# Kernel optimization log

Hardware: AMD Instinct MI355X
Metric: run time of the kernel (lower is better)

Reference implementation:

```python
import jax, jax.numpy as jnp
import numpy as np

# Model config (mirrors Mamba2Block(dim=256) with mamba_ssm defaults)
D_MODEL = 256
EXPAND = 2
D_INNER = D_MODEL * EXPAND          # 512
HEADDIM = D_MODEL * EXPAND // 8     # 64
NHEADS = D_INNER // HEADDIM         # 8
D_STATE = 64
D_CONV = 4
CONV_DIM = D_INNER + 2 * D_STATE    # 640 (ngroups=1)
D_IN_PROJ = 2 * D_INNER + 2 * D_STATE + NHEADS  # 1160
BATCH, SEQLEN = 2, 2048
EPS = 1e-5


def setup_inputs() -> dict:
    key = jax.random.key(0)
    ks = jax.random.split(key, 12)
    s = 0.02
    return {
        "hidden_states": jax.random.normal(ks[0], (BATCH, SEQLEN, D_MODEL), jnp.float32),
        "norm_w": jnp.ones((D_MODEL,), jnp.float32),
        "norm_b": jnp.zeros((D_MODEL,), jnp.float32),
        "W_in": jax.random.normal(ks[1], (D_MODEL, D_IN_PROJ), jnp.float32) * s,
        "conv_w": jax.random.normal(ks[2], (CONV_DIM, D_CONV), jnp.float32) * 0.25,
        "conv_b": jnp.zeros((CONV_DIM,), jnp.float32),
        "dt_bias": jax.random.uniform(ks[3], (NHEADS,), jnp.float32),
        "A_log": jax.random.uniform(ks[4], (NHEADS,), jnp.float32),  # A = -exp(A_log) in (-e, -1]
        "D_param": jnp.ones((NHEADS,), jnp.float32),
        "rms_w": jnp.ones((D_INNER,), jnp.float32),
        "W_out": jax.random.normal(ks[5], (D_INNER, D_MODEL), jnp.float32) * s,
    }


def _layer_norm(x, w, b):
    mu = jnp.mean(x, -1, keepdims=True)
    var = jnp.mean((x - mu) ** 2, -1, keepdims=True)
    return (x - mu) * jax.lax.rsqrt(var + EPS) * w + b


def _causal_depthwise_conv(x, w, b):
    # x: [B,L,C], w: [C,K] depthwise causal conv
    B, L, C = x.shape
    K = w.shape[1]
    xp = jnp.pad(x, ((0, 0), (K - 1, 0), (0, 0)))
    y = b
    for k in range(K):  # K=4, fixed small kernel
        y = y + w[:, k] * xp[:, k:k + L, :]
    return y


def reference(hidden_states, norm_w, norm_b, W_in, conv_w, conv_b, dt_bias, A_log, D_param, rms_w, W_out):
    B, L, D = hidden_states.shape
    residual = hidden_states                       # residual is None, drop_path=0
    x = _layer_norm(residual, norm_w, norm_b)      # pre-norm

    zxbcdt = jnp.einsum("bld,de->ble", x, W_in)    # [B,L,2*Di+2*N+H]
    z = zxbcdt[..., :D_INNER]
    xBC = zxbcdt[..., D_INNER:D_INNER + CONV_DIM]
    dt = zxbcdt[..., -NHEADS:]

    xBC = jax.nn.silu(_causal_depthwise_conv(xBC, conv_w, conv_b))
    xs = xBC[..., :D_INNER]
    Bm = xBC[..., D_INNER:D_INNER + D_STATE]       # [B,L,N] (ngroups=1)
    Cm = xBC[..., D_INNER + D_STATE:]              # [B,L,N]

    dt = jax.nn.softplus(dt + dt_bias)             # [B,L,H]
    A = -jnp.exp(A_log)                            # [H]
    dA = jnp.exp(dt * A)                           # [B,L,H]

    xh = xs.reshape(B, L, NHEADS, HEADDIM)         # [B,L,H,P]
    dtx = dt[..., None] * xh                       # [B,L,H,P]

    def step(s, inp):
        dA_t, dtx_t, B_t, C_t = inp                # [B,H],[B,H,P],[B,N],[B,N]
        s = s * dA_t[:, :, None, None] + dtx_t[..., None] * B_t[:, None, None, :]
        y_t = jnp.einsum("bhpn,bn->bhp", s, C_t)
        return s, y_t

    s0 = jnp.zeros((B, NHEADS, HEADDIM, D_STATE), hidden_states.dtype)
    xs_in = (jnp.swapaxes(dA, 0, 1), jnp.swapaxes(dtx, 0, 1),
             jnp.swapaxes(Bm, 0, 1), jnp.swapaxes(Cm, 0, 1))
    _, ys = jax.lax.scan(step, s0, xs_in)          # ys: [L,B,H,P]
    y = jnp.swapaxes(ys, 0, 1) + D_param[None, None, :, None] * xh  # skip term
    y = y.reshape(B, L, D_INNER)

    # gated RMSNorm (norm_before_gate=False): rmsnorm(y * silu(z)) * rms_w
    g = y * jax.nn.silu(z)
    g = g * jax.lax.rsqrt(jnp.mean(g * g, -1, keepdims=True) + EPS) * rms_w

    out = jnp.einsum("bld,de->ble", g, W_out)
    return out, residual
```

## Files before the change

kernel.cpp:

```cpp
#include <hip/hip_runtime.h>
#include <hip/hip_bf16.h>

#define BATCH 2
#define SEQLEN 2048
#define DMODEL 256
#define DINNER 512
#define NHEADS 8
#define HEADDIM 64
#define DSTATE 64
#define CONVDIM 640
#define DINPROJ 1160
#define NTOK (BATCH*SEQLEN)
#define Q 64
#define NCH (SEQLEN/Q)
#define NPAD2 1280
#define TS 72
#define RS3 196

typedef short v8s __attribute__((ext_vector_type(8)));
typedef float v4f __attribute__((ext_vector_type(4)));

__device__ __forceinline__ unsigned short f2bf(float f){
    __hip_bfloat16 h = __float2bfloat16(f);
    return *reinterpret_cast<unsigned short*>(&h);
}
__device__ __forceinline__ float bf2f(unsigned short u){
    unsigned int x = ((unsigned int)u) << 16;
    return __uint_as_float(x);
}

__global__ __launch_bounds__(256) void k_prep(
        const float* __restrict__ hid, const float* __restrict__ nw, const float* __restrict__ nb,
        const float* __restrict__ Win, const float* __restrict__ Wout,
        float* __restrict__ res, unsigned short* __restrict__ Xb,
        unsigned short* __restrict__ Wti, unsigned short* __restrict__ Wto){
    int bx = blockIdx.x;
    int t = threadIdx.x;
    if(bx < 256){
        __shared__ float xs[16][DMODEL];
        int tok0 = bx*16;
        for(int i=0;i<16;i++){
            int idx = i*256+t; int j = idx>>8, c = idx&255;
            float v = hid[(size_t)(tok0+j)*DMODEL + c];
            xs[j][c] = v;
            res[(size_t)(tok0+j)*DMODEL + c] = v;
        }
        __syncthreads();
        int g = t>>4, il = t&15;
        float sum=0.f, sumsq=0.f;
        for(int i=0;i<16;i++){ float v = xs[g][il*16+i]; sum += v; sumsq += v*v; }
        #pragma unroll
        for(int m=1;m<16;m<<=1){ sum += __shfl_xor(sum,m); sumsq += __shfl_xor(sumsq,m); }
        float mu   = sum*(1.f/256.f);
        float var  = sumsq*(1.f/256.f) - mu*mu;
        float rstd = rsqrtf(var + 1e-5f);
        for(int i=0;i<16;i++){
            int c = il*16+i;
            xs[g][c] = (xs[g][c]-mu)*rstd*nw[c] + nb[c];
        }
        __syncthreads();
        for(int i=0;i<16;i++){
            int idx = i*256+t; int j = idx>>8, c = idx&255;
            Xb[(size_t)(tok0+j)*DMODEL + c] = f2bf(xs[j][c]);
        }
    } else if(bx < 256 + NPAD2/4){
        int n0 = (bx-256)*4, k = t;
        #pragma unroll
        for(int i=0;i<4;i++){
            int n = n0+i;
            float v = (n < DINPROJ) ? Win[(size_t)k*DINPROJ + n] : 0.f;
            Wti[(size_t)n*DMODEL + k] = f2bf(v);
        }
    } else {
        int n0 = (bx - 256 - NPAD2/4)*4;
        #pragma unroll
        for(int kk=0;kk<2;kk++){
            int k = t + kk*256;
            #pragma unroll
            for(int i=0;i<4;i++){
                int n = n0+i;
                Wto[(size_t)n*DINNER + k] = f2bf(Wout[(size_t)k*DMODEL + n]);
            }
        }
    }
}

__global__ __launch_bounds__(256) void k_gemm_in(
        const unsigned short* __restrict__ A, const unsigned short* __restrict__ Bt,
        unsigned short* __restrict__ zxb){
    __shared__ __align__(16) unsigned short As[128*32];
    __shared__ __align__(16) unsigned short Bs[128*32];
    int t = threadIdx.x;
    int lane = t & 63, w = t >> 6;
    int lanelow = lane & 15, quad = lane >> 4;
    int tok0 = blockIdx.x * 128;
    int n0   = blockIdx.y * 128;
    int rw = (w & 1) * 64, cw = (w >> 1) * 64;
    v4f acc[4][4];
    #pragma unroll
    for(int mi=0;mi<4;mi++)
        #pragma unroll
        for(int ni=0;ni<4;ni++)
            acc[mi][ni] = (v4f){0.f,0.f,0.f,0.f};
    for(int k0=0; k0<DMODEL; k0+=32){
        __syncthreads();
        #pragma unroll
        for(int cc=0; cc<2; cc++){
            int u = t + cc*256;
            int row = u>>2, off = u&3;
            *(uint4*)&As[row*32 + off*8] = *(const uint4*)(A + (size_t)(tok0+row)*DMODEL + k0 + off*8);
            *(uint4*)&Bs[row*32 + off*8] = *(const uint4*)(Bt + (size_t)(n0+row)*DMODEL + k0 + off*8);
        }
        __syncthreads();
        v8s a[4], b[4];
        #pragma unroll
        for(int mi=0;mi<4;mi++) a[mi] = *(const v8s*)&As[(rw + mi*16 + lanelow)*32 + quad*8];
        #pragma unroll
        for(int ni=0;ni<4;ni++) b[ni] = *(const v8s*)&Bs[(cw + ni*16 + lanelow)*32 + quad*8];
        #pragma unroll
        for(int mi=0;mi<4;mi++)
            #pragma unroll
            for(int ni=0;ni<4;ni++)
                acc[mi][ni] = __builtin_amdgcn_mfma_f32_16x16x32_bf16(a[mi], b[ni], acc[mi][ni], 0,0,0);
    }
    #pragma unroll
    for(int mi=0;mi<4;mi++){
        #pragma unroll
        for(int ni=0;ni<4;ni++){
            int col = n0 + cw + ni*16 + lanelow;
            if(col < DINPROJ){
                #pragma unroll
                for(int r=0;r<4;r++){
                    int row = tok0 + rw + mi*16 + quad*4 + r;
                    zxb[(size_t)row*DINPROJ + col] = f2bf(acc[mi][ni][r]);
                }
            }
        }
    }
}

__global__ __launch_bounds__(256) void k_gemm_out(
        const unsigned short* __restrict__ Gb, const unsigned short* __restrict__ Wto,
        float* __restrict__ out){
    __shared__ __align__(16) unsigned short As[64*32];
    __shared__ __align__(16) unsigned short Bs[64*32];
    int t = threadIdx.x;
    int lane = t & 63, w = t >> 6;
    int lanelow = lane & 15, quad = lane >> 4;
    int tok0 = blockIdx.x * 64;
    int n0   = blockIdx.y * 64;
    v4f acc[4];
    #pragma unroll
    for(int ni=0;ni<4;ni++) acc[ni] = (v4f){0.f,0.f,0.f,0.f};
    for(int k0=0; k0<DINNER; k0+=32){
        __syncthreads();
        {
            int row = t>>2, off = t&3;
            *(uint4*)&As[row*32 + off*8] = *(const uint4*)(Gb + (size_t)(tok0+row)*DINNER + k0 + off*8);
            *(uint4*)&Bs[row*32 + off*8] = *(const uint4*)(Wto + (size_t)(n0+row)*DINNER + k0 + off*8);
        }
        __syncthreads();
        v8s a = *(const v8s*)&As[(w*16 + lanelow)*32 + quad*8];
        #pragma unroll
        for(int ni=0;ni<4;ni++){
            v8s b = *(const v8s*)&Bs[(ni*16 + lanelow)*32 + quad*8];
            acc[ni] = __builtin_amdgcn_mfma_f32_16x16x32_bf16(a, b, acc[ni], 0,0,0);
        }
    }
    #pragma unroll
    for(int ni=0;ni<4;ni++){
        int col = n0 + ni*16 + lanelow;
        #pragma unroll
        for(int r=0;r<4;r++){
            int row = tok0 + w*16 + quad*4 + r;
            out[(size_t)row*DMODEL + col] = acc[ni][r];
        }
    }
}

__global__ __launch_bounds__(256) void k_chunk1(
        const unsigned short* __restrict__ zxb, const float* __restrict__ conv_w, const float* __restrict__ conv_b,
        const float* __restrict__ dt_bias, const float* __restrict__ A_log, const float* __restrict__ D_param,
        unsigned short* __restrict__ yw16, unsigned short* __restrict__ contrib16,
        float* __restrict__ Larr, float* __restrict__ decayArr, unsigned short* __restrict__ Ccv){
    int blk = blockIdx.x;
    int c = blk & 31, h = (blk>>5)&7, b = blk>>8;
    int t = threadIdx.x;
    int lane = t & 63, w = t >> 6;
    int lanelow = lane & 15, quad = lane >> 4;
    __shared__ __align__(16) unsigned short Cb[64*TS];
    __shared__ __align__(16) unsigned short Bb[64*TS];
    __shared__ __align__(16) unsigned short BtW[64*TS];
    __shared__ __align__(16) unsigned short Xt[64*TS];
    __shared__ __align__(16) unsigned short Gbuf[64*TS];
    __shared__ __align__(16) unsigned short raw[19*RS3];
    __shared__ float Ls[Q], dts[Q], wch[Q];
    int l0 = c*Q;
    int bh = b*NHEADS + h;
    const unsigned short* zbase = zxb + (size_t)(b*SEQLEN + l0)*DINPROJ;
    if(t < Q){
        float v = bf2f(zbase[(size_t)t*DINPROJ + (DINPROJ-NHEADS) + h]) + dt_bias[h];
        float dt = (v > 20.f) ? v : log1pf(__expf(v));
        float A  = -__expf(A_log[h]);
        float ld = dt*A;
        #pragma unroll
        for(int off=1; off<64; off<<=1){
            float u = __shfl_up(ld, off);
            if(lane >= off) ld += u;
        }
        Ls[t] = ld; dts[t] = dt;
    }
    __syncthreads();
    float L63 = Ls[Q-1];
    if(t < Q) wch[t] = __expf(L63 - Ls[t]) * dts[t];
    unsigned short* CcP = Ccv + ((size_t)b*NCH + c)*4096;
    for(int s=0; s<4; s++){
        __syncthreads();
        #pragma unroll
        for(int i=0;i<4;i++){
            int u = t + 256*i;
            if(u < 19*48){
                int row = u/48, seg = u%48;
                int l = l0 + s*16 - 3 + row;
                int gcol = (seg<16) ? (DINNER + h*HEADDIM + seg*4) : (2*DINNER + (seg-16)*4);
                ushort4 v;
                if(l >= 0) v = *(const ushort4*)(zxb + ((size_t)b*SEQLEN + l)*DINPROJ + gcol);
                else { v.x=0; v.y=0; v.z=0; v.w=0; }
                *(ushort4*)&raw[row*RS3 + seg*4] = v;
            }
        }
        __syncthreads();
        #pragma unroll
        for(int i=0;i<3;i++){
            int u = t + 256*i;
            int stl = u & 15, grp = u >> 4;
            int st = s*16 + stl;
            int ch = grp*4;
            float xk[4][4];
            #pragma unroll
            for(int k=0;k<4;k++){
                ushort4 v = *(const ushort4*)&raw[(stl+k)*RS3 + ch];
                xk[k][0]=bf2f(v.x); xk[k][1]=bf2f(v.y); xk[k][2]=bf2f(v.z); xk[k][3]=bf2f(v.w);
            }
            float wst = wch[st];
            #pragma unroll
            for(int j=0;j<4;j++){
                int chj = ch+j;
                int cc = (chj<64) ? (h*HEADDIM + chj) : (448 + chj);
                float4 wv = *(const float4*)&conv_w[cc*4];
                float acc = conv_b[cc] + wv.x*xk[0][j] + wv.y*xk[1][j] + wv.z*xk[2][j] + wv.w*xk[3][j];
                float sv = acc/(1.f+__expf(-acc));
                if(chj < 64){
                    Xt[chj*TS + st] = f2bf(sv);
                } else if(chj < 128){
                    int n = chj-64;
                    Bb[st*TS + n]  = f2bf(sv);
                    BtW[n*TS + st] = f2bf(sv*wst);
                } else {
                    int n = chj-128;
                    unsigned short sb16 = f2bf(sv);
                    Cb[st*TS + n] = sb16;
                    if(h==0) CcP[st*64 + n] = sb16;
                }
            }
        }
    }
    __syncthreads();
    v4f g[4];
    #pragma unroll
    for(int nt=0;nt<4;nt++) g[nt] = (v4f){0.f,0.f,0.f,0.f};
    #pragma unroll
    for(int kk=0;kk<2;kk++){
        v8s a = *(const v8s*)&Cb[(w*16+lanelow)*TS + kk*32 + quad*8];
        #pragma unroll
        for(int nt=0;nt<4;nt++){
            v8s bb = *(const v8s*)&Bb[(nt*16+lanelow)*TS + kk*32 + quad*8];
            g[nt] = __builtin_amdgcn_mfma_f32_16x16x32_bf16(a, bb, g[nt], 0,0,0);
        }
    }
    float Lrow[4];
    #pragma unroll
    for(int r=0;r<4;r++) Lrow[r] = Ls[w*16 + quad*4 + r];
    #pragma unroll
    for(int nt=0;nt<4;nt++){
        int col = nt*16 + lanelow;
        float Lc = Ls[col], dtc = dts[col];
        #pragma unroll
        for(int r=0;r<4;r++){
            int rowg = w*16 + quad*4 + r;
            float val = (col <= rowg) ? g[nt][r] * __expf(Lrow[r]-Lc) * dtc : 0.f;
            Gbuf[rowg*TS + col] = f2bf(val);
        }
    }
    __syncthreads();
    v4f ya[4], sa[4];
    #pragma unroll
    for(int nt=0;nt<4;nt++){ ya[nt]=(v4f){0.f,0.f,0.f,0.f}; sa[nt]=(v4f){0.f,0.f,0.f,0.f}; }
    #pragma unroll
    for(int kk=0;kk<2;kk++){
        v8s ag = *(const v8s*)&Gbuf[(w*16+lanelow)*TS + kk*32 + quad*8];
        v8s ax = *(const v8s*)&Xt[(w*16+lanelow)*TS + kk*32 + quad*8];
        #pragma unroll
        for(int nt=0;nt<4;nt++){
            v8s bx = *(const v8s*)&Xt[(nt*16+lanelow)*TS + kk*32 + quad*8];
            v8s bw = *(const v8s*)&BtW[(nt*16+lanelow)*TS + kk*32 + quad*8];
            ya[nt] = __builtin_amdgcn_mfma_f32_16x16x32_bf16(ag, bx, ya[nt], 0,0,0);
            sa[nt] = __builtin_amdgcn_mfma_f32_16x16x32_bf16(ax, bw, sa[nt], 0,0,0);
        }
    }
    float Dp = D_param[h];
    #pragma unroll
    for(int nt=0;nt<4;nt++){
        int col = nt*16 + lanelow;
        #pragma unroll
        for(int r=0;r<4;r++){
            int i = w*16 + quad*4 + r;
            float xval = bf2f(Xt[col*TS + i]);
            yw16[((size_t)b*SEQLEN + l0 + i)*DINNER + h*HEADDIM + col] = f2bf(ya[nt][r] + Dp*xval);
            contrib16[(((size_t)bh*NCH + c)*64 + i)*64 + col] = f2bf(sa[nt][r]);
        }
    }
    if(t < Q) Larr[((size_t)bh*NCH + c)*Q + t] = Ls[t];
    if(t == 0) decayArr[bh*NCH + c] = __expf(L63);
}

__global__ __launch_bounds__(256) void k_chunk2(const unsigned short* __restrict__ contrib16,
                                                const float* __restrict__ decayArr,
                                                unsigned short* __restrict__ Sb){
    int bh = blockIdx.x >> 4;
    int part = blockIdx.x & 15;
    int e = part*256 + threadIdx.x;
    const size_t base = (size_t)bh*NCH*4096 + e;
    float vals[NCH];
    #pragma unroll
    for(int c=0;c<NCH;c++) vals[c] = bf2f(contrib16[base + (size_t)c*4096]);
    float s = 0.f;
    #pragma unroll
    for(int c=0;c<NCH;c++){
        Sb[base + (size_t)c*4096] = f2bf(s);
        s = fmaf(s, decayArr[bh*NCH + c], vals[c]);
    }
}

__global__ __launch_bounds__(512) void k_tail(
        const unsigned short* __restrict__ Ccv, const unsigned short* __restrict__ Sb,
        const float* __restrict__ Larr, const unsigned short* __restrict__ yw16,
        const unsigned short* __restrict__ zxb, const float* __restrict__ rms_w,
        unsigned short* __restrict__ Gb){
    int blk = blockIdx.x;
    int q4 = blk & 3, c = (blk>>2) & 31, b = blk >> 7;
    int t = threadIdx.x;
    int h = t >> 6, lane = t & 63;
    int lanelow = lane & 15, quad = lane >> 4;
    int bh = b*NHEADS + h;
    __shared__ float wsum[8][16];
    __shared__ float rstdS[16];
    const unsigned short* Cp = Ccv + ((size_t)b*NCH + c)*4096;
    const unsigned short* Sp = Sb + ((size_t)bh*NCH + c)*4096;
    int row0 = q4*16;
    v8s a0 = *(const v8s*)(Cp + (row0+lanelow)*64 + quad*8);
    v8s a1 = *(const v8s*)(Cp + (row0+lanelow)*64 + 32 + quad*8);
    v8s s[4][2];
    #pragma unroll
    for(int nt=0;nt<4;nt++){
        s[nt][0] = *(const v8s*)(Sp + (nt*16+lanelow)*64 + quad*8);
        s[nt][1] = *(const v8s*)(Sp + (nt*16+lanelow)*64 + 32 + quad*8);
    }
    float g[4][4];
    float sq[4] = {0.f,0.f,0.f,0.f};
    const float* Lp = Larr + ((size_t)bh*NCH + c)*Q;
    float eL[4];
    #pragma unroll
    for(int r=0;r<4;r++) eL[r] = __expf(Lp[row0 + quad*4 + r]);
    #pragma unroll
    for(int nt=0;nt<4;nt++){
        v4f acc = (v4f){0.f,0.f,0.f,0.f};
        acc = __builtin_amdgcn_mfma_f32_16x16x32_bf16(a0, s[nt][0], acc, 0,0,0);
        acc = __builtin_amdgcn_mfma_f32_16x16x32_bf16(a1, s[nt][1], acc, 0,0,0);
        int col = h*HEADDIM + nt*16 + lanelow;
        #pragma unroll
        for(int r=0;r<4;r++){
            int i = row0 + quad*4 + r;
            size_t tok = (size_t)b*SEQLEN + c*Q + i;
            float yv = acc[r]*eL[r] + bf2f(yw16[tok*DINNER + col]);
            float z  = bf2f(zxb[tok*DINPROJ + col]);
            float gg = yv * (z/(1.f+__expf(-z)));
            g[nt][r] = gg;
            sq[r] += gg*gg;
        }
    }
    #pragma unroll
    for(int r=0;r<4;r++){
        float v = sq[r];
        #pragma unroll
        for(int m=1;m<16;m<<=1) v += __shfl_xor(v, m);
        sq[r] = v;
    }
    if(lanelow==0){
        #pragma unroll
        for(int r=0;r<4;r++) wsum[h][quad*4 + r] = sq[r];
    }
    __syncthreads();
    if(t < 16){
        float tot = 0.f;
        #pragma unroll
        for(int hh=0;hh<8;hh++) tot += wsum[hh][t];
        rstdS[t] = rsqrtf(tot*(1.f/512.f) + 1e-5f);
    }
    __syncthreads();
    #pragma unroll
    for(int nt=0;nt<4;nt++){
        int col = h*HEADDIM + nt*16 + lanelow;
        float rw = rms_w[col];
        #pragma unroll
        for(int r=0;r<4;r++){
            int i = row0 + quad*4 + r;
            Gb[((size_t)b*SEQLEN + c*Q + i)*DINNER + col] = f2bf(g[nt][r] * rstdS[quad*4 + r] * rw);
        }
    }
}

extern "C" void kernel_launch(void* const* d_in, const int* in_sizes, int n_in,
                              void* d_out, int out_size, void* d_ws, size_t ws_size,
                              hipStream_t stream) {
    const float* hid     = (const float*)d_in[0];
    const float* norm_w  = (const float*)d_in[1];
    const float* norm_b  = (const float*)d_in[2];
    const float* Win     = (const float*)d_in[3];
    const float* conv_w  = (const float*)d_in[4];
    const float* conv_b  = (const float*)d_in[5];
    const float* dt_bias = (const float*)d_in[6];
    const float* A_log   = (const float*)d_in[7];
    const float* D_param = (const float*)d_in[8];
    const float* rms_w   = (const float*)d_in[9];
    const float* Wout    = (const float*)d_in[10];

    unsigned short* contrib16 = (unsigned short*)d_ws;
    float* Larr    = (float*)(contrib16 + (size_t)16*NCH*4096);
    float* decayA  = Larr + (size_t)16*NCH*Q;
    unsigned short* zxb  = (unsigned short*)(decayA + 512);
    unsigned short* yw16 = zxb + (size_t)NTOK*DINPROJ;
    unsigned short* Sb   = yw16 + (size_t)NTOK*DINNER;
    unsigned short* Ccv  = Sb + (size_t)16*NCH*4096;
    unsigned short* Xb   = Ccv + (size_t)BATCH*NCH*4096;
    unsigned short* Gb   = Xb + (size_t)NTOK*DMODEL;
    unsigned short* Wti  = Gb + (size_t)NTOK*DINNER;
    unsigned short* Wto  = Wti + (size_t)NPAD2*DMODEL;

    float* out = (float*)d_out;
    float* res = out + (size_t)NTOK*DMODEL;

    k_prep<<<256 + NPAD2/4 + DMODEL/4, 256, 0, stream>>>(hid, norm_w, norm_b, Win, Wout, res, Xb, Wti, Wto);
    k_gemm_in<<<dim3(NTOK/128, NPAD2/128), 256, 0, stream>>>(Xb, Wti, zxb);
    k_chunk1<<<BATCH*NHEADS*NCH, 256, 0, stream>>>(zxb, conv_w, conv_b, dt_bias, A_log, D_param,
                                                   yw16, contrib16, Larr, decayA, Ccv);
    k_chunk2<<<256, 256, 0, stream>>>(contrib16, decayA, Sb);
    k_tail<<<BATCH*NCH*4, 512, 0, stream>>>(Ccv, Sb, Larr, yw16, zxb, rms_w, Gb);
    k_gemm_out<<<dim3(NTOK/64, DMODEL/64), 256, 0, stream>>>(Gb, Wto, out);
}
```

Baseline: 129.4 us.

## Fuse output projection into gated-RMSNorm tail kernel and fold rms_w into W_out

Measured after the change: 129.0 us. Within noise of the previous version (-0.3%).

```diff
diff --git a/kernel.cpp b/kernel.cpp
--- a/kernel.cpp
+++ b/kernel.cpp
@@ -31,7 +31,7 @@
 
 __global__ __launch_bounds__(256) void k_prep(
         const float* __restrict__ hid, const float* __restrict__ nw, const float* __restrict__ nb,
-        const float* __restrict__ Win, const float* __restrict__ Wout,
+        const float* __restrict__ Win, const float* __restrict__ Wout, const float* __restrict__ rms_w,
         float* __restrict__ res, unsigned short* __restrict__ Xb,
         unsigned short* __restrict__ Wti, unsigned short* __restrict__ Wto){
     int bx = blockIdx.x;
@@ -76,10 +76,11 @@
         #pragma unroll
         for(int kk=0;kk<2;kk++){
             int k = t + kk*256;
+            float rw = rms_w[k];
             #pragma unroll
             for(int i=0;i<4;i++){
                 int n = n0+i;
-                Wto[(size_t)n*DINNER + k] = f2bf(Wout[(size_t)k*DMODEL + n]);
+                Wto[(size_t)n*DINNER + k] = f2bf(Wout[(size_t)k*DMODEL + n] * rw);
             }
         }
     }
@@ -135,45 +136,6 @@
                     zxb[(size_t)row*DINPROJ + col] = f2bf(acc[mi][ni][r]);
                 }
             }
-        }
-    }
-}
-
-__global__ __launch_bounds__(256) void k_gemm_out(
-        const unsigned short* __restrict__ Gb, const unsigned short* __restrict__ Wto,
-        float* __restrict__ out){
-    __shared__ __align__(16) unsigned short As[64*32];
-    __shared__ __align__(16) unsigned short Bs[64*32];
-    int t = threadIdx.x;
-    int lane = t & 63, w = t >> 6;
-    int lanelow = lane & 15, quad = lane >> 4;
-    int tok0 = blockIdx.x * 64;
-    int n0   = blockIdx.y * 64;
-    v4f acc[4];
-    #pragma unroll
-    for(int ni=0;ni<4;ni++) acc[ni] = (v4f){0.f,0.f,0.f,0.f};
-    for(int k0=0; k0<DINNER; k0+=32){
-        __syncthreads();
-        {
-            int row = t>>2, off = t&3;
-            *(uint4*)&As[row*32 + off*8] = *(const uint4*)(Gb + (size_t)(tok0+row)*DINNER + k0 + off*8);
-            *(uint4*)&Bs[row*32 + off*8] = *(const uint4*)(Wto + (size_t)(n0+row)*DINNER + k0 + off*8);
-        }
-        __syncthreads();
-        v8s a = *(const v8s*)&As[(w*16 + lanelow)*32 + quad*8];
-        #pragma unroll
-        for(int ni=0;ni<4;ni++){
-            v8s b = *(const v8s*)&Bs[(ni*16 + lanelow)*32 + quad*8];
-            acc[ni] = __builtin_amdgcn_mfma_f32_16x16x32_bf16(a, b, acc[ni], 0,0,0);
-        }
-    }
-    #pragma unroll
-    for(int ni=0;ni<4;ni++){
-        int col = n0 + ni*16 + lanelow;
-        #pragma unroll
-        for(int r=0;r<4;r++){
-            int row = tok0 + w*16 + quad*4 + r;
-            out[(size_t)row*DMODEL + col] = acc[ni][r];
         }
     }
 }
@@ -345,14 +307,15 @@
 __global__ __launch_bounds__(512) void k_tail(
         const unsigned short* __restrict__ Ccv, const unsigned short* __restrict__ Sb,
         const float* __restrict__ Larr, const unsigned short* __restrict__ yw16,
-        const unsigned short* __restrict__ zxb, const float* __restrict__ rms_w,
-        unsigned short* __restrict__ Gb){
+        const unsigned short* __restrict__ zxb, const unsigned short* __restrict__ Wto,
+        float* __restrict__ out){
     int blk = blockIdx.x;
     int q4 = blk & 3, c = (blk>>2) & 31, b = blk >> 7;
     int t = threadIdx.x;
     int h = t >> 6, lane = t & 63;
     int lanelow = lane & 15, quad = lane >> 4;
     int bh = b*NHEADS + h;
+    __shared__ __align__(16) unsigned short Gs[16*528];
     __shared__ float wsum[8][16];
     __shared__ float rstdS[16];
     const unsigned short* Cp = Ccv + ((size_t)b*NCH + c)*4096;
@@ -366,12 +329,12 @@
         s[nt][0] = *(const v8s*)(Sp + (nt*16+lanelow)*64 + quad*8);
         s[nt][1] = *(const v8s*)(Sp + (nt*16+lanelow)*64 + 32 + quad*8);
     }
-    float g[4][4];
     float sq[4] = {0.f,0.f,0.f,0.f};
     const float* Lp = Larr + ((size_t)bh*NCH + c)*Q;
     float eL[4];
     #pragma unroll
     for(int r=0;r<4;r++) eL[r] = __expf(Lp[row0 + quad*4 + r]);
+    size_t tok0 = (size_t)b*SEQLEN + c*Q + row0;
     #pragma unroll
     for(int nt=0;nt<4;nt++){
         v4f acc = (v4f){0.f,0.f,0.f,0.f};
@@ -380,12 +343,11 @@
         int col = h*HEADDIM + nt*16 + lanelow;
         #pragma unroll
         for(int r=0;r<4;r++){
-            int i = row0 + quad*4 + r;
-            size_t tok = (size_t)b*SEQLEN + c*Q + i;
+            size_t tok = tok0 + quad*4 + r;
             float yv = acc[r]*eL[r] + bf2f(yw16[tok*DINNER + col]);
             float z  = bf2f(zxb[tok*DINPROJ + col]);
             float gg = yv * (z/(1.f+__expf(-z)));
-            g[nt][r] = gg;
+            Gs[(quad*4+r)*528 + col] = f2bf(gg);
             sq[r] += gg*gg;
         }
     }
@@ -408,15 +370,26 @@
         rstdS[t] = rsqrtf(tot*(1.f/512.f) + 1e-5f);
     }
     __syncthreads();
-    #pragma unroll
-    for(int nt=0;nt<4;nt++){
-        int col = h*HEADDIM + nt*16 + lanelow;
-        float rw = rms_w[col];
-        #pragma unroll
-        for(int r=0;r<4;r++){
-            int i = row0 + quad*4 + r;
-            Gb[((size_t)b*SEQLEN + c*Q + i)*DINNER + col] = f2bf(g[nt][r] * rstdS[quad*4 + r] * rw);
-        }
+    v4f acc2[2];
+    #pragma unroll
+    for(int nt=0;nt<2;nt++) acc2[nt] = (v4f){0.f,0.f,0.f,0.f};
+    for(int ki=0; ki<16; ki++){
+        v8s a = *(const v8s*)&Gs[lanelow*528 + ki*32 + quad*8];
+        #pragma unroll
+        for(int nt=0;nt<2;nt++){
+            v8s bfr = *(const v8s*)(Wto + (size_t)(h*32 + nt*16 + lanelow)*DINNER + ki*32 + quad*8);
+            acc2[nt] = __builtin_amdgcn_mfma_f32_16x16x32_bf16(a, bfr, acc2[nt], 0,0,0);
+        }
+    }
+    float rs[4];
+    #pragma unroll
+    for(int r=0;r<4;r++) rs[r] = rstdS[quad*4 + r];
+    #pragma unroll
+    for(int nt=0;nt<2;nt++){
+        int col = h*32 + nt*16 + lanelow;
+        #pragma unroll
+        for(int r=0;r<4;r++)
+            out[(tok0 + quad*4 + r)*DMODEL + col] = acc2[nt][r]*rs[r];
     }
 }
 
@@ -443,18 +416,16 @@
     unsigned short* Sb   = yw16 + (size_t)NTOK*DINNER;
     unsigned short* Ccv  = Sb + (size_t)16*NCH*4096;
     unsigned short* Xb   = Ccv + (size_t)BATCH*NCH*4096;
-    unsigned short* Gb   = Xb + (size_t)NTOK*DMODEL;
-    unsigned short* Wti  = Gb + (size_t)NTOK*DINNER;
+    unsigned short* Wti  = Xb + (size_t)NTOK*DMODEL;
     unsigned short* Wto  = Wti + (size_t)NPAD2*DMODEL;
 
     float* out = (float*)d_out;
     float* res = out + (size_t)NTOK*DMODEL;
 
-    k_prep<<<256 + NPAD2/4 + DMODEL/4, 256, 0, stream>>>(hid, norm_w, norm_b, Win, Wout, res, Xb, Wti, Wto);
+    k_prep<<<256 + NPAD2/4 + DMODEL/4, 256, 0, stream>>>(hid, norm_w, norm_b, Win, Wout, rms_w, res, Xb, Wti, Wto);
     k_gemm_in<<<dim3(NTOK/128, NPAD2/128), 256, 0, stream>>>(Xb, Wti, zxb);
     k_chunk1<<<BATCH*NHEADS*NCH, 256, 0, stream>>>(zxb, conv_w, conv_b, dt_bias, A_log, D_param,
                                                    yw16, contrib16, Larr, decayA, Ccv);
     k_chunk2<<<256, 256, 0, stream>>>(contrib16, decayA, Sb);
-    k_tail<<<BATCH*NCH*4, 512, 0, stream>>>(Ccv, Sb, Larr, yw16, zxb, rms_w, Gb);
-    k_gemm_out<<<dim3(NTOK/64, DMODEL/64), 256, 0, stream>>>(Gb, Wto, out);
-}
+    k_tail<<<BATCH*NCH*4, 512, 0, stream>>>(Ccv, Sb, Larr, yw16, zxb, Wto, out);
+}
```
